# Optimization experiments

Hardware: AMD Instinct MI355X
Metric: run time of the kernel (lower is better)

The kernel has to match this reference:

```python
import jax, jax.numpy as jnp
import numpy as np

HIDDEN = 1024
N_EXPERTS = 8
TOP_K = 2
INTER = 1408
NORM_TOPK = False


def setup_inputs() -> dict:
    key = jax.random.key(0)
    ks = jax.random.split(key, 5)
    B, S = 4, 2048
    scale_h = 1.0 / np.sqrt(HIDDEN)
    scale_i = 1.0 / np.sqrt(INTER)
    return {
        "hidden_states": jax.random.normal(ks[0], (B, S, HIDDEN), dtype=jnp.float32),
        "gate_w": jax.random.normal(ks[1], (N_EXPERTS, HIDDEN), dtype=jnp.float32) * scale_h,  # router
        "w_gate": jax.random.normal(ks[2], (N_EXPERTS, HIDDEN, INTER), dtype=jnp.float32) * scale_h,
        "w_up": jax.random.normal(ks[3], (N_EXPERTS, HIDDEN, INTER), dtype=jnp.float32) * scale_h,
        "w_down": jax.random.normal(ks[4], (N_EXPERTS, INTER, HIDDEN), dtype=jnp.float32) * scale_i,
    }


def reference(hidden_states, gate_w, w_gate, w_up, w_down):
    B, S, H = hidden_states.shape
    x = hidden_states.reshape(-1, H)                     # [T, H]
    T = x.shape[0]

    router_logits = x @ gate_w.T                          # [T, E]
    probs = jax.nn.softmax(router_logits.astype(jnp.float32), axis=-1)
    topk_w, topk_idx = jax.lax.top_k(probs, TOP_K)        # [T, K]
    if NORM_TOPK:
        topk_w = topk_w / jnp.sum(topk_w, axis=-1, keepdims=True)
    topk_w = topk_w.astype(x.dtype)

    # Scatter top-k weights into dense [T, E] combine weights (0 for unselected).
    weights = jnp.zeros((T, N_EXPERTS), dtype=x.dtype)
    weights = weights.at[jnp.arange(T)[:, None], topk_idx].set(topk_w)

    # Dense grouped SwiGLU over all experts; combine masks out unrouted pairs.
    g = jnp.einsum('th,ehi->eti', x, w_gate)              # [E, T, I]
    u = jnp.einsum('th,ehi->eti', x, w_up)                # [E, T, I]
    y = jnp.einsum('eti,eih->eth', jax.nn.silu(g) * u, w_down)  # [E, T, H]
    final = jnp.einsum('eth,te->th', y, weights)          # [T, H]

    return final.reshape(B, S, H), router_logits
```

## Files before the change

### kernel.cpp

```cpp
#include <hip/hip_runtime.h>
#include <hip/hip_bf16.h>
#include <math.h>

#define T_TOK 8192
#define HID   1024
#define NE    8
#define TOPKN 2
#define INTER 1408
#define NROWS (T_TOK*TOPKN)
#define MAXWL 144
#define RBLK  256

typedef __attribute__((ext_vector_type(8))) __bf16 bf16x8;
typedef __attribute__((ext_vector_type(4))) float f32x4;
typedef __attribute__((ext_vector_type(4))) unsigned int u32x4;

__device__ __forceinline__ unsigned short f2bf(float f) {
    unsigned int u = __builtin_bit_cast(unsigned int, f);
    unsigned int lsb = (u >> 16) & 1u;
    u += 0x7fffu + lsb;
    return (unsigned short)(u >> 16);
}

__device__ __forceinline__ void gl2lds16(const void* g, void* l) {
    __builtin_amdgcn_global_load_lds(
        (const __attribute__((address_space(1))) unsigned int*)g,
        (__attribute__((address_space(3))) unsigned int*)l, 16, 0, 0);
}

__global__ __launch_bounds__(256) void moe_router(
    const float* __restrict__ x, const float* __restrict__ gate_w,
    unsigned short* __restrict__ xb, float* __restrict__ logits_out,
    int* __restrict__ topk_idx, float* __restrict__ topk_w,
    int* __restrict__ hist_g)
{
    __shared__ int lh[NE];
    int tid = threadIdx.x, wave = tid >> 6, lane = tid & 63;
    if (tid < NE) lh[tid] = 0;
    __syncthreads();

#pragma unroll 1
    for (int i = 0; i < 8; i++) {
        int t = blockIdx.x * 32 + wave * 8 + i;
        const float4* xr = (const float4*)(x + (size_t)t * HID);
        float acc[NE];
#pragma unroll
        for (int e = 0; e < NE; e++) acc[e] = 0.f;
#pragma unroll
        for (int j = 0; j < 4; j++) {
            float4 xv = xr[j * 64 + lane];
            ushort4 pk;
            pk.x = f2bf(xv.x); pk.y = f2bf(xv.y);
            pk.z = f2bf(xv.z); pk.w = f2bf(xv.w);
            *(ushort4*)(xb + (size_t)t * HID + j * 256 + lane * 4) = pk;
#pragma unroll
            for (int e = 0; e < NE; e++) {
                float4 gv = *(const float4*)(gate_w + e * HID + j * 256 + lane * 4);
                acc[e] += xv.x * gv.x + xv.y * gv.y + xv.z * gv.z + xv.w * gv.w;
            }
        }
#pragma unroll
        for (int e = 0; e < NE; e++) {
            float v = acc[e];
#pragma unroll
            for (int off = 32; off; off >>= 1) v += __shfl_xor(v, off, 64);
            acc[e] = v;
        }
        if (lane == 0) {
            float m = acc[0];
#pragma unroll
            for (int e = 1; e < NE; e++) m = fmaxf(m, acc[e]);
            float p[NE]; float s = 0.f;
#pragma unroll
            for (int e = 0; e < NE; e++) { p[e] = expf(acc[e] - m); s += p[e]; }
            float inv = 1.f / s;
#pragma unroll
            for (int e = 0; e < NE; e++) logits_out[(size_t)t * NE + e] = acc[e];
            int i0 = 0;
#pragma unroll
            for (int e = 1; e < NE; e++) if (p[e] > p[i0]) i0 = e;
            int i1 = (i0 == 0) ? 1 : 0;
#pragma unroll
            for (int e = 0; e < NE; e++) if (e != i0 && p[e] > p[i1]) i1 = e;
            topk_idx[2 * t]     = i0; topk_w[2 * t]     = p[i0] * inv;
            topk_idx[2 * t + 1] = i1; topk_w[2 * t + 1] = p[i1] * inv;
            atomicAdd(&lh[i0], 1);
            atomicAdd(&lh[i1], 1);
        }
    }
    __syncthreads();
    if (tid < NE) hist_g[blockIdx.x * NE + tid] = lh[tid];
}

__global__ __launch_bounds__(256) void moe_scan(
    const int* __restrict__ hist_g, int* __restrict__ offsets,
    int* __restrict__ block_base, int* __restrict__ wl, int* __restrict__ n_wl)
{
    __shared__ int h[RBLK * NE];
    __shared__ int cnt[NE], offs[NE];
    int tid = threadIdx.x;
    for (int i = tid; i < RBLK * NE; i += 256) h[i] = hist_g[i];
    __syncthreads();
    if (tid < NE) {
        int s = 0;
        for (int b = 0; b < RBLK; b++) s += h[b * NE + tid];
        cnt[tid] = s;
    }
    __syncthreads();
    if (tid == 0) {
        int s = 0;
        for (int e = 0; e < NE; e++) { offs[e] = s; offsets[e] = s; s += cnt[e]; }
        offsets[NE] = s;
        int n = 0;
        for (int e = 0; e < NE; e++)
            for (int r0 = 0; r0 < cnt[e]; r0 += 128)
                wl[n++] = (e << 24) | r0;
        *n_wl = n;
    }
    __syncthreads();
    if (tid < NE) {
        int run = offs[tid];
        for (int b = 0; b < RBLK; b++) {
            block_base[b * NE + tid] = run;
            run += h[b * NE + tid];
        }
    }
}

__global__ __launch_bounds__(64) void moe_scatter(
    const int* __restrict__ topk_idx, const float* __restrict__ topk_w,
    const int* __restrict__ block_base, int* __restrict__ row_token,
    float* __restrict__ row_w, int* __restrict__ tok_rows)
{
    __shared__ int base[NE];
    int tid = threadIdx.x;
    if (tid < NE) base[tid] = block_base[blockIdx.x * NE + tid];
    __syncthreads();
    int idx = blockIdx.x * 64 + tid;
    int e = topk_idx[idx];
    int pos = atomicAdd(&base[e], 1);
    row_token[pos] = idx >> 1;
    row_w[pos] = topk_w[idx];
    tok_rows[idx] = pos;
}

__global__ __launch_bounds__(256) void moe_transpose_cast(
    const float* __restrict__ in, unsigned short* __restrict__ out,
    int R_, int C_)
{
    __shared__ float tile[32][33];
    int e = blockIdx.z;
    const float* ine = in + (size_t)e * R_ * C_;
    unsigned short* oute = out + (size_t)e * R_ * C_;
    int c0 = blockIdx.x * 32, r0 = blockIdx.y * 32;
    int tx = threadIdx.x, ty = threadIdx.y;
#pragma unroll
    for (int j = 0; j < 4; j++) {
        int r = r0 + ty + j * 8;
        tile[ty + j * 8][tx] = ine[(size_t)r * C_ + c0 + tx];
    }
    __syncthreads();
#pragma unroll
    for (int j = 0; j < 4; j++) {
        int c = c0 + ty + j * 8;
        oute[(size_t)c * R_ + r0 + tx] = f2bf(tile[tx][ty + j * 8]);
    }
}

__global__ __launch_bounds__(256) void moe_gemm1(
    const unsigned short* __restrict__ xb,
    const unsigned short* __restrict__ wg_t,
    const unsigned short* __restrict__ wu_t,
    const int* __restrict__ offsets, const int* __restrict__ row_token,
    const int* __restrict__ wl, const int* __restrict__ n_wl,
    unsigned short* __restrict__ h_buf)
{
    if ((int)blockIdx.y >= *n_wl) return;
    int wle = wl[blockIdx.y];
    int e = wle >> 24, row0 = wle & 0xffffff;
    int off = offsets[e], cnt = offsets[e + 1] - off;
    int i0 = blockIdx.x * 64;

    __shared__ __align__(16) unsigned short As[128 * 64];
    __shared__ __align__(16) unsigned short Bg[64 * 64];
    __shared__ __align__(16) unsigned short Bu[64 * 64];

    int tid = threadIdx.x, wave = tid >> 6, lane = tid & 63;
    int wm = wave & 1, wn = wave >> 1;
    int l16 = lane & 15, quad = lane >> 4;
    int r_ = lane >> 3, c_ = lane & 7;
    int sw = l16 & 7;

    const unsigned short* asrc[4];
#pragma unroll
    for (int it = 0; it < 4; it++) {
        int rloc = it * 32 + wave * 8 + r_;
        int rg = row0 + rloc;
        int tok = row_token[off + ((rg < cnt) ? rg : 0)];
        asrc[it] = xb + (size_t)tok * HID + (c_ ^ (rloc & 7)) * 8;
    }
    const unsigned short* bgsrc[2];
    const unsigned short* busrc[2];
#pragma unroll
    for (int it = 0; it < 2; it++) {
        int rloc = it * 32 + wave * 8 + r_;
        size_t boff = (size_t)e * INTER * HID + (size_t)(i0 + rloc) * HID + (c_ ^ (rloc & 7)) * 8;
        bgsrc[it] = wg_t + boff;
        busrc[it] = wu_t + boff;
    }

    f32x4 accg[4][2], accu[4][2];
#pragma unroll
    for (int mi = 0; mi < 4; mi++)
#pragma unroll
        for (int ni = 0; ni < 2; ni++) {
            accg[mi][ni] = {0.f, 0.f, 0.f, 0.f};
            accu[mi][ni] = {0.f, 0.f, 0.f, 0.f};
        }

    for (int k0 = 0; k0 < HID; k0 += 64) {
#pragma unroll
        for (int it = 0; it < 4; it++)
            gl2lds16(asrc[it] + k0, &As[(it * 32 + wave * 8) * 64]);
#pragma unroll
        for (int it = 0; it < 2; it++) {
            gl2lds16(bgsrc[it] + k0, &Bg[(it * 32 + wave * 8) * 64]);
            gl2lds16(busrc[it] + k0, &Bu[(it * 32 + wave * 8) * 64]);
        }
        __syncthreads();
#pragma unroll
        for (int kk8 = 0; kk8 < 8; kk8 += 4) {
            int q = kk8 + quad;
            int qs = (q ^ sw) * 8;
            bf16x8 a[4], bg[2], bu[2];
#pragma unroll
            for (int mi = 0; mi < 4; mi++)
                a[mi] = *(const bf16x8*)&As[(wm * 64 + mi * 16 + l16) * 64 + qs];
#pragma unroll
            for (int ni = 0; ni < 2; ni++) {
                bg[ni] = *(const bf16x8*)&Bg[(wn * 32 + ni * 16 + l16) * 64 + qs];
                bu[ni] = *(const bf16x8*)&Bu[(wn * 32 + ni * 16 + l16) * 64 + qs];
            }
#pragma unroll
            for (int mi = 0; mi < 4; mi++)
#pragma unroll
                for (int ni = 0; ni < 2; ni++) {
                    accg[mi][ni] = __builtin_amdgcn_mfma_f32_16x16x32_bf16(a[mi], bg[ni], accg[mi][ni], 0, 0, 0);
                    accu[mi][ni] = __builtin_amdgcn_mfma_f32_16x16x32_bf16(a[mi], bu[ni], accu[mi][ni], 0, 0, 0);
                }
        }
        __syncthreads();
    }
#pragma unroll
    for (int mi = 0; mi < 4; mi++)
#pragma unroll
        for (int ni = 0; ni < 2; ni++)
#pragma unroll
            for (int r = 0; r < 4; r++) {
                int ml = wm * 64 + mi * 16 + quad * 4 + r;
                int row = row0 + ml;
                if (row < cnt) {
                    float g = accg[mi][ni][r], u = accu[mi][ni][r];
                    float hv = (g / (1.f + expf(-g))) * u;
                    h_buf[(size_t)(off + row) * INTER + i0 + wn * 32 + ni * 16 + l16] = f2bf(hv);
                }
            }
}

__global__ __launch_bounds__(256) void moe_gemm2(
    const unsigned short* __restrict__ h_buf,
    const unsigned short* __restrict__ wd_t,
    const int* __restrict__ offsets, const float* __restrict__ row_w,
    const int* __restrict__ wl, const int* __restrict__ n_wl,
    unsigned short* __restrict__ y_buf)
{
    if ((int)blockIdx.y >= *n_wl) return;
    int wle = wl[blockIdx.y];
    int e = wle >> 24, row0 = wle & 0xffffff;
    int off = offsets[e], cnt = offsets[e + 1] - off;
    int h0 = blockIdx.x * 128;

    __shared__ __align__(16) unsigned short As[128 * 64];
    __shared__ __align__(16) unsigned short Bs[128 * 64];

    int tid = threadIdx.x, wave = tid >> 6, lane = tid & 63;
    int wm = wave & 1, wn = wave >> 1;
    int l16 = lane & 15, quad = lane >> 4;
    int r_ = lane >> 3, c_ = lane & 7;
    int sw = l16 & 7;

    const unsigned short* asrc[4];
    const unsigned short* bsrc[4];
#pragma unroll
    for (int it = 0; it < 4; it++) {
        int rloc = it * 32 + wave * 8 + r_;
        int rg = row0 + rloc;
        asrc[it] = h_buf + (size_t)(off + ((rg < cnt) ? rg : 0)) * INTER + (c_ ^ (rloc & 7)) * 8;
        bsrc[it] = wd_t + (size_t)e * HID * INTER + (size_t)(h0 + rloc) * INTER + (c_ ^ (rloc & 7)) * 8;
    }

    f32x4 acc[4][4];
#pragma unroll
    for (int mi = 0; mi < 4; mi++)
#pragma unroll
        for (int ni = 0; ni < 4; ni++) acc[mi][ni] = {0.f, 0.f, 0.f, 0.f};

    for (int k0 = 0; k0 < INTER; k0 += 64) {
#pragma unroll
        for (int it = 0; it < 4; it++) {
            gl2lds16(asrc[it] + k0, &As[(it * 32 + wave * 8) * 64]);
            gl2lds16(bsrc[it] + k0, &Bs[(it * 32 + wave * 8) * 64]);
        }
        __syncthreads();
#pragma unroll
        for (int kk8 = 0; kk8 < 8; kk8 += 4) {
            int q = kk8 + quad;
            int qs = (q ^ sw) * 8;
            bf16x8 a[4], b[4];
#pragma unroll
            for (int mi = 0; mi < 4; mi++)
                a[mi] = *(const bf16x8*)&As[(wm * 64 + mi * 16 + l16) * 64 + qs];
#pragma unroll
            for (int ni = 0; ni < 4; ni++)
                b[ni] = *(const bf16x8*)&Bs[(wn * 64 + ni * 16 + l16) * 64 + qs];
#pragma unroll
            for (int mi = 0; mi < 4; mi++)
#pragma unroll
                for (int ni = 0; ni < 4; ni++)
                    acc[mi][ni] = __builtin_amdgcn_mfma_f32_16x16x32_bf16(a[mi], b[ni], acc[mi][ni], 0, 0, 0);
        }
        __syncthreads();
    }
#pragma unroll
    for (int mi = 0; mi < 4; mi++)
#pragma unroll
        for (int ni = 0; ni < 4; ni++)
#pragma unroll
            for (int r = 0; r < 4; r++) {
                int ml = wm * 64 + mi * 16 + quad * 4 + r;
                int row = row0 + ml;
                if (row < cnt) {
                    float w = row_w[off + row];
                    y_buf[(size_t)(off + row) * HID + h0 + wn * 64 + ni * 16 + l16] =
                        f2bf(acc[mi][ni][r] * w);
                }
            }
}

__global__ __launch_bounds__(256) void moe_combine(
    const unsigned short* __restrict__ y_buf, const int* __restrict__ tok_rows,
    float* __restrict__ out)
{
    int gid = blockIdx.x * 256 + threadIdx.x;
    int t = gid >> 7;
    int c = gid & 127;
    u32x4 a = *(const u32x4*)(y_buf + (size_t)tok_rows[2 * t]     * HID + c * 8);
    u32x4 b = *(const u32x4*)(y_buf + (size_t)tok_rows[2 * t + 1] * HID + c * 8);
    float res[8];
#pragma unroll
    for (int j = 0; j < 4; j++) {
        unsigned int wa = a[j], wb = b[j];
        res[2 * j]     = __builtin_bit_cast(float, wa << 16)
                       + __builtin_bit_cast(float, wb << 16);
        res[2 * j + 1] = __builtin_bit_cast(float, wa & 0xffff0000u)
                       + __builtin_bit_cast(float, wb & 0xffff0000u);
    }
    float* o = out + (size_t)t * HID + c * 8;
    *(float4*)(o)     = make_float4(res[0], res[1], res[2], res[3]);
    *(float4*)(o + 4) = make_float4(res[4], res[5], res[6], res[7]);
}

extern "C" void kernel_launch(void* const* d_in, const int* in_sizes, int n_in,
                              void* d_out, int out_size, void* d_ws, size_t ws_size,
                              hipStream_t stream)
{
    const float* x      = (const float*)d_in[0];
    const float* gate_w = (const float*)d_in[1];
    const float* w_gate = (const float*)d_in[2];
    const float* w_up   = (const float*)d_in[3];
    const float* w_down = (const float*)d_in[4];
    float* out = (float*)d_out;
    float* logits_out = out + (size_t)T_TOK * HID;

    char* ws = (char*)d_ws;
    int*   offsets    = (int*)(ws + 0);
    int*   n_wl       = (int*)(ws + 64);
    int*   wl         = (int*)(ws + 128);
    int*   hist_g     = (int*)(ws + 1024);
    int*   block_base = (int*)(ws + 1024 + 8192);
    int*   topk_idx   = (int*)(ws + 32768);
    float* topk_w     = (float*)(ws + 32768 + 65536);
    int*   row_token  = (int*)(ws + 32768 + 2 * 65536);
    float* row_w      = (float*)(ws + 32768 + 3 * 65536);
    int*   tok_rows   = (int*)(ws + 32768 + 4 * 65536);
    size_t o = 32768 + 5 * (size_t)65536 + 32768;
    unsigned short* xb   = (unsigned short*)(ws + o); o += (size_t)T_TOK * HID * 2;
    unsigned short* wg_t = (unsigned short*)(ws + o); o += (size_t)NE * INTER * HID * 2;
    unsigned short* wu_t = (unsigned short*)(ws + o); o += (size_t)NE * INTER * HID * 2;
    unsigned short* wd_t = (unsigned short*)(ws + o); o += (size_t)NE * HID * INTER * 2;
    unsigned short* h_buf = (unsigned short*)(ws + o); o += (size_t)NROWS * INTER * 2;
    unsigned short* y_buf = (unsigned short*)(ws + o); o += (size_t)NROWS * HID * 2;

    moe_router<<<RBLK, 256, 0, stream>>>(x, gate_w, xb, logits_out,
                                         topk_idx, topk_w, hist_g);
    moe_scan<<<1, 256, 0, stream>>>(hist_g, offsets, block_base, wl, n_wl);
    moe_scatter<<<RBLK, 64, 0, stream>>>(topk_idx, topk_w, block_base,
                                         row_token, row_w, tok_rows);
    dim3 tb(32, 8, 1);
    moe_transpose_cast<<<dim3(INTER / 32, HID / 32, NE), tb, 0, stream>>>(w_gate, wg_t, HID, INTER);
    moe_transpose_cast<<<dim3(INTER / 32, HID / 32, NE), tb, 0, stream>>>(w_up,   wu_t, HID, INTER);
    moe_transpose_cast<<<dim3(HID / 32, INTER / 32, NE), tb, 0, stream>>>(w_down, wd_t, INTER, HID);

    moe_gemm1<<<dim3(INTER / 64, MAXWL), 256, 0, stream>>>(
        xb, wg_t, wu_t, offsets, row_token, wl, n_wl, h_buf);
    moe_gemm2<<<dim3(HID / 128, MAXWL), 256, 0, stream>>>(
        h_buf, wd_t, offsets, row_w, wl, n_wl, y_buf);
    moe_combine<<<(T_TOK * HID / 8) / 256, 256, 0, stream>>>(y_buf, tok_rows, out);
}
```

Before: 470.9 us.

## Double-buffer GEMM LDS tiles, vectorize weight transpose, parallelize scan counts

Both grouped GEMM kernels now use two LDS buffers, so the next K-tile's global-to-LDS load is issued before computing on the current tile, and one barrier per tile is dropped. The weight transpose-cast kernel uses 64x64 tiles with float4 loads and packed ushort4 stores, which cuts the number of memory transactions. The scan kernel sums per-expert histograms with 32 lanes per expert and a shuffle reduction instead of one serial thread per expert. The cost is twice the LDS per GEMM block, which may lower occupancy.

```diff
diff --git a/kernel.cpp b/kernel.cpp
--- a/kernel.cpp
+++ b/kernel.cpp
@@ -101,10 +101,13 @@
     int tid = threadIdx.x;
     for (int i = tid; i < RBLK * NE; i += 256) h[i] = hist_g[i];
     __syncthreads();
-    if (tid < NE) {
+    {
+        int e = tid >> 5, g = tid & 31;
         int s = 0;
-        for (int b = 0; b < RBLK; b++) s += h[b * NE + tid];
-        cnt[tid] = s;
+        for (int b = g; b < RBLK; b += 32) s += h[b * NE + e];
+#pragma unroll
+        for (int off2 = 16; off2; off2 >>= 1) s += __shfl_xor(s, off2, 32);
+        if (g == 0) cnt[e] = s;
     }
     __syncthreads();
     if (tid == 0) {
@@ -148,22 +151,32 @@
     const float* __restrict__ in, unsigned short* __restrict__ out,
     int R_, int C_)
 {
-    __shared__ float tile[32][33];
+    __shared__ float tile[64][65];
     int e = blockIdx.z;
     const float* ine = in + (size_t)e * R_ * C_;
     unsigned short* oute = out + (size_t)e * R_ * C_;
-    int c0 = blockIdx.x * 32, r0 = blockIdx.y * 32;
-    int tx = threadIdx.x, ty = threadIdx.y;
+    int c0 = blockIdx.x * 64, r0 = blockIdx.y * 64;
+    int tid = threadIdx.x;
+    int lr = tid >> 4;
+    int lc = tid & 15;
 #pragma unroll
     for (int j = 0; j < 4; j++) {
-        int r = r0 + ty + j * 8;
-        tile[ty + j * 8][tx] = ine[(size_t)r * C_ + c0 + tx];
+        int r = lr + j * 16;
+        float4 v = *(const float4*)(ine + (size_t)(r0 + r) * C_ + c0 + lc * 4);
+        tile[r][lc * 4 + 0] = v.x; tile[r][lc * 4 + 1] = v.y;
+        tile[r][lc * 4 + 2] = v.z; tile[r][lc * 4 + 3] = v.w;
     }
     __syncthreads();
 #pragma unroll
     for (int j = 0; j < 4; j++) {
-        int c = c0 + ty + j * 8;
-        oute[(size_t)c * R_ + r0 + tx] = f2bf(tile[tx][ty + j * 8]);
+        int c = (tid >> 4) + j * 16;
+        int r = (tid & 15) * 4;
+        ushort4 pk;
+        pk.x = f2bf(tile[r + 0][c]);
+        pk.y = f2bf(tile[r + 1][c]);
+        pk.z = f2bf(tile[r + 2][c]);
+        pk.w = f2bf(tile[r + 3][c]);
+        *(ushort4*)(oute + (size_t)(c0 + c) * R_ + r0 + r) = pk;
     }
 }
 
@@ -181,9 +194,9 @@
     int off = offsets[e], cnt = offsets[e + 1] - off;
     int i0 = blockIdx.x * 64;
 
-    __shared__ __align__(16) unsigned short As[128 * 64];
-    __shared__ __align__(16) unsigned short Bg[64 * 64];
-    __shared__ __align__(16) unsigned short Bu[64 * 64];
+    __shared__ __align__(16) unsigned short As[2][128 * 64];
+    __shared__ __align__(16) unsigned short Bg[2][64 * 64];
+    __shared__ __align__(16) unsigned short Bu[2][64 * 64];
 
     int tid = threadIdx.x, wave = tid >> 6, lane = tid & 63;
     int wm = wave & 1, wn = wave >> 1;
@@ -218,16 +231,18 @@
             accu[mi][ni] = {0.f, 0.f, 0.f, 0.f};
         }
 
-    for (int k0 = 0; k0 < HID; k0 += 64) {
+    auto stage = [&](unsigned short* asb, unsigned short* bgb, unsigned short* bub, int k0) {
 #pragma unroll
         for (int it = 0; it < 4; it++)
-            gl2lds16(asrc[it] + k0, &As[(it * 32 + wave * 8) * 64]);
+            gl2lds16(asrc[it] + k0, asb + (it * 32 + wave * 8) * 64);
 #pragma unroll
         for (int it = 0; it < 2; it++) {
-            gl2lds16(bgsrc[it] + k0, &Bg[(it * 32 + wave * 8) * 64]);
-            gl2lds16(busrc[it] + k0, &Bu[(it * 32 + wave * 8) * 64]);
-        }
-        __syncthreads();
+            gl2lds16(bgsrc[it] + k0, bgb + (it * 32 + wave * 8) * 64);
+            gl2lds16(busrc[it] + k0, bub + (it * 32 + wave * 8) * 64);
+        }
+    };
+    auto compute = [&](const unsigned short* asb, const unsigned short* bgb,
+                       const unsigned short* bub) {
 #pragma unroll
         for (int kk8 = 0; kk8 < 8; kk8 += 4) {
             int q = kk8 + quad;
@@ -235,11 +250,11 @@
             bf16x8 a[4], bg[2], bu[2];
 #pragma unroll
             for (int mi = 0; mi < 4; mi++)
-                a[mi] = *(const bf16x8*)&As[(wm * 64 + mi * 16 + l16) * 64 + qs];
+                a[mi] = *(const bf16x8*)&asb[(wm * 64 + mi * 16 + l16) * 64 + qs];
 #pragma unroll
             for (int ni = 0; ni < 2; ni++) {
-                bg[ni] = *(const bf16x8*)&Bg[(wn * 32 + ni * 16 + l16) * 64 + qs];
-                bu[ni] = *(const bf16x8*)&Bu[(wn * 32 + ni * 16 + l16) * 64 + qs];
+                bg[ni] = *(const bf16x8*)&bgb[(wn * 32 + ni * 16 + l16) * 64 + qs];
+                bu[ni] = *(const bf16x8*)&bub[(wn * 32 + ni * 16 + l16) * 64 + qs];
             }
 #pragma unroll
             for (int mi = 0; mi < 4; mi++)
@@ -249,8 +264,20 @@
                     accu[mi][ni] = __builtin_amdgcn_mfma_f32_16x16x32_bf16(a[mi], bu[ni], accu[mi][ni], 0, 0, 0);
                 }
         }
+    };
+
+    stage(As[0], Bg[0], Bu[0], 0);
+    __syncthreads();
+#pragma unroll 1
+    for (int t = 0; t < 16; t += 2) {
+        stage(As[1], Bg[1], Bu[1], (t + 1) * 64);
+        compute(As[0], Bg[0], Bu[0]);
         __syncthreads();
-    }
+        if (t + 2 < 16) stage(As[0], Bg[0], Bu[0], (t + 2) * 64);
+        compute(As[1], Bg[1], Bu[1]);
+        __syncthreads();
+    }
+
 #pragma unroll
     for (int mi = 0; mi < 4; mi++)
 #pragma unroll
@@ -280,8 +307,8 @@
     int off = offsets[e], cnt = offsets[e + 1] - off;
     int h0 = blockIdx.x * 128;
 
-    __shared__ __align__(16) unsigned short As[128 * 64];
-    __shared__ __align__(16) unsigned short Bs[128 * 64];
+    __shared__ __align__(16) unsigned short As[2][128 * 64];
+    __shared__ __align__(16) unsigned short Bs[2][128 * 64];
 
     int tid = threadIdx.x, wave = tid >> 6, lane = tid & 63;
     int wm = wave & 1, wn = wave >> 1;
@@ -305,13 +332,14 @@
 #pragma unroll
         for (int ni = 0; ni < 4; ni++) acc[mi][ni] = {0.f, 0.f, 0.f, 0.f};
 
-    for (int k0 = 0; k0 < INTER; k0 += 64) {
+    auto stage = [&](unsigned short* asb, unsigned short* bsb, int k0) {
 #pragma unroll
         for (int it = 0; it < 4; it++) {
-            gl2lds16(asrc[it] + k0, &As[(it * 32 + wave * 8) * 64]);
-            gl2lds16(bsrc[it] + k0, &Bs[(it * 32 + wave * 8) * 64]);
-        }
-        __syncthreads();
+            gl2lds16(asrc[it] + k0, asb + (it * 32 + wave * 8) * 64);
+            gl2lds16(bsrc[it] + k0, bsb + (it * 32 + wave * 8) * 64);
+        }
+    };
+    auto compute = [&](const unsigned short* asb, const unsigned short* bsb) {
 #pragma unroll
         for (int kk8 = 0; kk8 < 8; kk8 += 4) {
             int q = kk8 + quad;
@@ -319,18 +347,30 @@
             bf16x8 a[4], b[4];
 #pragma unroll
             for (int mi = 0; mi < 4; mi++)
-                a[mi] = *(const bf16x8*)&As[(wm * 64 + mi * 16 + l16) * 64 + qs];
+                a[mi] = *(const bf16x8*)&asb[(wm * 64 + mi * 16 + l16) * 64 + qs];
 #pragma unroll
             for (int ni = 0; ni < 4; ni++)
-                b[ni] = *(const bf16x8*)&Bs[(wn * 64 + ni * 16 + l16) * 64 + qs];
+                b[ni] = *(const bf16x8*)&bsb[(wn * 64 + ni * 16 + l16) * 64 + qs];
 #pragma unroll
             for (int mi = 0; mi < 4; mi++)
 #pragma unroll
                 for (int ni = 0; ni < 4; ni++)
                     acc[mi][ni] = __builtin_amdgcn_mfma_f32_16x16x32_bf16(a[mi], b[ni], acc[mi][ni], 0, 0, 0);
         }
+    };
+
+    stage(As[0], Bs[0], 0);
+    __syncthreads();
+#pragma unroll 1
+    for (int t = 0; t < 22; t += 2) {
+        stage(As[1], Bs[1], (t + 1) * 64);
+        compute(As[0], Bs[0]);
         __syncthreads();
-    }
+        if (t + 2 < 22) stage(As[0], Bs[0], (t + 2) * 64);
+        compute(As[1], Bs[1]);
+        __syncthreads();
+    }
+
 #pragma unroll
     for (int mi = 0; mi < 4; mi++)
 #pragma unroll
@@ -406,10 +446,9 @@
     moe_scan<<<1, 256, 0, stream>>>(hist_g, offsets, block_base, wl, n_wl);
     moe_scatter<<<RBLK, 64, 0, stream>>>(topk_idx, topk_w, block_base,
                                          row_token, row_w, tok_rows);
-    dim3 tb(32, 8, 1);
-    moe_transpose_cast<<<dim3(INTER / 32, HID / 32, NE), tb, 0, stream>>>(w_gate, wg_t, HID, INTER);
-    moe_transpose_cast<<<dim3(INTER / 32, HID / 32, NE), tb, 0, stream>>>(w_up,   wu_t, HID, INTER);
-    moe_transpose_cast<<<dim3(HID / 32, INTER / 32, NE), tb, 0, stream>>>(w_down, wd_t, INTER, HID);
+    moe_transpose_cast<<<dim3(INTER / 64, HID / 64, NE), 256, 0, stream>>>(w_gate, wg_t, HID, INTER);
+    moe_transpose_cast<<<dim3(INTER / 64, HID / 64, NE), 256, 0, stream>>>(w_up,   wu_t, HID, INTER);
+    moe_transpose_cast<<<dim3(HID / 64, INTER / 64, NE), 256, 0, stream>>>(w_down, wd_t, INTER, HID);
 
     moe_gemm1<<<dim3(INTER / 64, MAXWL), 256, 0, stream>>>(
         xb, wg_t, wu_t, offsets, row_token, wl, n_wl, h_buf);
```

Measured after the change: 468.0 us. Within noise of the previous version (-0.6%).
